# Kernel tuning notes

Measured on AMD Instinct MI355X. Metric: run time of the kernel, lower is better.

Reference implementation:

```python
import jax, jax.numpy as jnp
import numpy as np

N = 100_000      # nodes
E = 1_600_000    # edges
D = 128          # in_dim == hidden_dim
H = 4            # heads
HD = D // H      # per-head dim = 32
B = 8            # graphs in batch
TD = 128         # time_dim
NEG_SLOPE = 0.2
EPS = 1e-5


def _gelu(v):
    return jax.nn.gelu(v, approximate=False)  # torch default erf-GELU


def _layernorm(v, g, b):
    mu = jnp.mean(v, axis=-1, keepdims=True)
    var = jnp.var(v, axis=-1, keepdims=True)
    return (v - mu) * jax.lax.rsqrt(var + EPS) * g + b


def setup_inputs() -> dict:
    key = jax.random.key(0)
    ks = jax.random.split(key, 24)
    s = 1.0 / np.sqrt(D)
    inp = {
        "x": jax.random.normal(ks[0], (N, D), jnp.float32),
        "src": jax.random.randint(ks[1], (E,), 0, N),
        "dst": jax.random.randint(ks[2], (E,), 0, N),
        "graph_ids": jnp.sort(jax.random.randint(ks[3], (N,), 0, B)),
        "time_emb": jax.random.normal(ks[4], (B, TD), jnp.float32),
        # GATv2 params
        "Wsrc": jax.random.normal(ks[5], (D, D), jnp.float32) * s,
        "bsrc": jnp.zeros((D,), jnp.float32),
        "Wdst": jax.random.normal(ks[6], (D, D), jnp.float32) * s,
        "bdst": jnp.zeros((D,), jnp.float32),
        "attn": jax.random.normal(ks[7], (H, HD), jnp.float32) * (1.0 / np.sqrt(HD)),
        "gat_bias": jnp.zeros((D,), jnp.float32),
        # LayerNorms
        "ln1_g": jnp.ones((D,), jnp.float32), "ln1_b": jnp.zeros((D,), jnp.float32),
        "ln2_g": jnp.ones((D,), jnp.float32), "ln2_b": jnp.zeros((D,), jnp.float32),
        # time MLP
        "tW": jax.random.normal(ks[8], (TD, D), jnp.float32) * (1.0 / np.sqrt(TD)),
        "tb": jnp.zeros((D,), jnp.float32),
        # FFN
        "W1": jax.random.normal(ks[9], (D, 2 * D), jnp.float32) * s,
        "b1": jnp.zeros((2 * D,), jnp.float32),
        "W2": jax.random.normal(ks[10], (2 * D, D), jnp.float32) * (1.0 / np.sqrt(2 * D)),
        "b2": jnp.zeros((D,), jnp.float32),
    }
    return inp


def reference(x, src, dst, graph_ids, time_emb, Wsrc, bsrc, Wdst, bdst, attn,
              gat_bias, ln1_g, ln1_b, ln2_g, ln2_b, tW, tb, W1, b1, W2, b2):
    h = _layernorm(x, ln1_g, ln1_b)                       # [N, D]
    # GATv2Conv (share_weights=False, residual=False, activation=gelu)
    feat_src = (h @ Wsrc + bsrc).reshape(N, H, HD)        # [N, H, HD]
    feat_dst = (h @ Wdst + bdst).reshape(N, H, HD)
    e = feat_src[src] + feat_dst[dst]                     # [E, H, HD]
    e = jnp.where(e > 0, e, NEG_SLOPE * e)                # leaky_relu
    scores = jnp.einsum("ehd,hd->eh", e, attn)            # [E, H]
    # segment softmax over incoming edges of each dst node
    m = jax.ops.segment_max(scores, dst, num_segments=N)  # [N, H]
    ex = jnp.exp(scores - m[dst])
    denom = jax.ops.segment_sum(ex, dst, num_segments=N)  # [N, H]
    alpha = ex / denom[dst]                               # [E, H]
    msg = feat_src[src] * alpha[:, :, None]               # [E, H, HD]
    rst = jax.ops.segment_sum(msg, dst, num_segments=N)   # [N, H, HD]
    rst = _gelu(rst + gat_bias.reshape(H, HD))
    h = rst.reshape(N, D)                                 # flatten(1)
    # ragged time-embedding expand: time_condition[graph_of(node)]
    time_cond = _gelu(time_emb @ tW + tb)                 # [B, D]
    h = h + time_cond[graph_ids]
    h = h + x                                             # proj = Identity (in_dim == hidden_dim)
    h2 = _layernorm(h, ln2_g, ln2_b)
    h2 = _gelu(h2 @ W1 + b1) @ W2 + b2                    # FFN
    return h + h2
```

## Files before the change

### kernel.cpp

```cpp
#include <hip/hip_runtime.h>
#include <hip/hip_bf16.h>


#define RB 16
#define NEG_SLOPE 0.2f
#define LN_EPS 1e-5f

typedef __attribute__((ext_vector_type(8))) short short8v;
typedef __attribute__((ext_vector_type(4))) float floatx4;
typedef __attribute__((ext_vector_type(2))) float f32x2;

__device__ __forceinline__ float gelu_erf(float v) {
    return 0.5f * v * (1.0f + erff(v * 0.70710678118654752f));
}
__device__ __forceinline__ unsigned short f2bf(float f) {
    unsigned int u = __float_as_uint(f);
    u += 0x7fffu + ((u >> 16) & 1u);
    return (unsigned short)(u >> 16);
}

__device__ __forceinline__ void pack_region(
    const float* __restrict__ W, unsigned short* __restrict__ P, int K, int C, int idx)
{
    int total = (K >> 5) * (C >> 4) * 64;
    if (idx >= total) return;
    int lane = idx & 63;
    int f = idx >> 6;
    int nkt = K >> 5;
    int nt = f / nkt, kt = f - nt * nkt;
    int col = nt * 16 + (lane & 15);
    int k0 = kt * 32 + 8 * (lane >> 4);
    short8v v;
    #pragma unroll
    for (int i = 0; i < 8; ++i)
        v[i] = (short)f2bf(W[(size_t)(k0 + i) * C + col]);
    *(short8v*)(P + (size_t)idx * 8) = v;
}

__global__ __launch_bounds__(256) void prep(
    const float* __restrict__ temb, const float* __restrict__ tW,
    const float* __restrict__ tb, float* __restrict__ tc, int B,
    const float* __restrict__ Wsrc, unsigned short* __restrict__ pWs,
    const float* __restrict__ Wdst, unsigned short* __restrict__ pWd,
    const float* __restrict__ W1,   unsigned short* __restrict__ pW1,
    const float* __restrict__ W2,   unsigned short* __restrict__ pW2,
    int* __restrict__ deg, int N)
{
    const int bid = blockIdx.x;
    const int t   = threadIdx.x;
    if (bid == 0) {
        __shared__ float te[8 * 128];
        for (int i = t; i < B * 128; i += 256) te[i] = temb[i];
        __syncthreads();
        int c = t & 127, half = t >> 7;
        for (int b = half * 4; b < half * 4 + 4; ++b) {
            if (b >= B) break;
            float acc = 0.f;
            for (int k = 0; k < 128; ++k) acc = fmaf(te[b * 128 + k], tW[k * 128 + c], acc);
            tc[b * 128 + c] = gelu_erf(acc + tb[c]);
        }
    } else if (bid < 9) {
        pack_region(Wsrc, pWs, 128, 128, (bid - 1) * 256 + t);
    } else if (bid < 17) {
        pack_region(Wdst, pWd, 128, 128, (bid - 9) * 256 + t);
    } else if (bid < 33) {
        pack_region(W1, pW1, 128, 256, (bid - 17) * 256 + t);
    } else if (bid < 49) {
        pack_region(W2, pW2, 256, 128, (bid - 33) * 256 + t);
    } else {
        int idx = (bid - 49) * 1024 + t * 4;
        if (idx + 3 < N) {
            *(int4*)(deg + idx) = make_int4(0, 0, 0, 0);
        } else {
            if (idx     < N) deg[idx]     = 0;
            if (idx + 1 < N) deg[idx + 1] = 0;
            if (idx + 2 < N) deg[idx + 2] = 0;
            if (idx + 3 < N) deg[idx + 3] = 0;
        }
    }
}

__global__ __launch_bounds__(256) void csr_rank(
    const int* __restrict__ dst, int* __restrict__ deg, int* __restrict__ rank, int E)
{
    int e = blockIdx.x * 256 + threadIdx.x;
    if (e < E) rank[e] = atomicAdd(&deg[dst[e]], 1);
}

__global__ __launch_bounds__(256) void scan_blocks(
    const int* __restrict__ deg, int* __restrict__ rs, int* __restrict__ btot, int N)
{
    __shared__ int wtot[4];
    const int t    = threadIdx.x;
    const int idx  = blockIdx.x * 1024 + t * 4;
    int d0 = 0, d1 = 0, d2 = 0, d3 = 0;
    if (idx + 3 < N) {
        int4 v = *(const int4*)(deg + idx);
        d0 = v.x; d1 = v.y; d2 = v.z; d3 = v.w;
    } else {
        if (idx     < N) d0 = deg[idx];
        if (idx + 1 < N) d1 = deg[idx + 1];
        if (idx + 2 < N) d2 = deg[idx + 2];
        if (idx + 3 < N) d3 = deg[idx + 3];
    }
    const int ts = d0 + d1 + d2 + d3;
    const int lane = t & 63, w = t >> 6;
    int incl = ts;
    #pragma unroll
    for (int m = 1; m < 64; m <<= 1) { int u = __shfl_up(incl, m); if (lane >= m) incl += u; }
    if (lane == 63) wtot[w] = incl;
    __syncthreads();
    int woff = 0;
    #pragma unroll
    for (int i = 0; i < 4; ++i) woff += (i < w) ? wtot[i] : 0;
    const int p = woff + incl - ts;
    if (idx + 3 < N) {
        int4 o;
        o.x = p; o.y = p + d0; o.z = p + d0 + d1; o.w = p + d0 + d1 + d2;
        *(int4*)(rs + idx) = o;
    } else {
        if (idx     < N) rs[idx]     = p;
        if (idx + 1 < N) rs[idx + 1] = p + d0;
        if (idx + 2 < N) rs[idx + 2] = p + d0 + d1;
        if (idx + 3 < N) rs[idx + 3] = p + d0 + d1 + d2;
    }
    if (t == 255) btot[blockIdx.x] = woff + incl;
}

__global__ __launch_bounds__(64) void scan_tops(
    int* __restrict__ btot, int nb, int* __restrict__ rs, int N, int E)
{
    const int lane = threadIdx.x;
    int a0 = (2 * lane     < nb) ? btot[2 * lane]     : 0;
    int a1 = (2 * lane + 1 < nb) ? btot[2 * lane + 1] : 0;
    const int ts = a0 + a1;
    int incl = ts;
    #pragma unroll
    for (int m = 1; m < 64; m <<= 1) { int u = __shfl_up(incl, m); if (lane >= m) incl += u; }
    const int ex = incl - ts;
    if (2 * lane     < nb) btot[2 * lane]     = ex;
    if (2 * lane + 1 < nb) btot[2 * lane + 1] = ex + a0;
    if (lane == 0) rs[N] = E;
}

__global__ __launch_bounds__(256) void scan_add(
    int* __restrict__ rs, const int* __restrict__ btot, int N)
{
    int i = blockIdx.x * 256 + threadIdx.x;
    if (i < N) rs[i] += btot[i >> 10];
}

__global__ __launch_bounds__(256) void ln1_fill(
    const float* __restrict__ x,
    const float* __restrict__ ln_g, const float* __restrict__ ln_b,
    const unsigned short* __restrict__ pWs, const float* __restrict__ bsrc,
    const unsigned short* __restrict__ pWd, const float* __restrict__ bdst,
    unsigned short* __restrict__ fs, unsigned short* __restrict__ fdB, int nrows, int nLn1,
    const int* __restrict__ dst, const int* __restrict__ srcA,
    const int* __restrict__ rs, const int* __restrict__ rank,
    int* __restrict__ srcSorted, int E)
{
    __shared__ __align__(16) float hs[RB][132];
    __shared__ __align__(16) unsigned short pa[4 * 64 * 8];
    __shared__ float s_mu[RB], s_rs[RB];

    if (blockIdx.x >= nLn1) {
        int e = (blockIdx.x - nLn1) * 256 + threadIdx.x;
        if (e < E) srcSorted[rs[dst[e]] + rank[e]] = srcA[e];
        return;
    }

    const int tid  = threadIdx.x;
    const int row0 = blockIdx.x * RB;
    const int lane = tid & 63;
    const int w    = tid >> 6;

    #pragma unroll
    for (int i = 0; i < 2; ++i) {
        int f   = tid + i * 256;
        int row = f >> 5;
        int c0  = (f & 31) * 4;
        float4 v = make_float4(0.f, 0.f, 0.f, 0.f);
        if (row0 + row < nrows) v = *(const float4*)(x + (size_t)(row0 + row) * 128 + c0);
        *(float4*)&hs[row][c0] = v;
    }
    __syncthreads();

    {
        const int ln = lane;
        #pragma unroll
        for (int rr = 0; rr < 4; ++rr) {
            int row = w * 4 + rr;
            float v0 = hs[row][ln * 2], v1 = hs[row][ln * 2 + 1];
            float s = v0 + v1, sq = v0 * v0 + v1 * v1;
            #pragma unroll
            for (int m = 32; m; m >>= 1) { s += __shfl_xor(s, m); sq += __shfl_xor(sq, m); }
            if (ln == 0) {
                float mu  = s * (1.0f / 128.0f);
                float var = sq * (1.0f / 128.0f) - mu * mu;
                s_mu[row] = mu;
                s_rs[row] = rsqrtf(var + LN_EPS);
            }
        }
    }
    __syncthreads();

    {
        const int kt  = w;
        const int row = lane & 15;
        const int k0  = kt * 32 + 8 * (lane >> 4);
        float mu = s_mu[row], rs2 = s_rs[row];
        float4 u  = *(float4*)&hs[row][k0];
        float4 v  = *(float4*)&hs[row][k0 + 4];
        float4 g0 = *(const float4*)&ln_g[k0];
        float4 g1 = *(const float4*)&ln_g[k0 + 4];
        float4 c0 = *(const float4*)&ln_b[k0];
        float4 c1 = *(const float4*)&ln_b[k0 + 4];
        short8v pv;
        pv[0] = (short)f2bf((u.x - mu) * rs2 * g0.x + c0.x);
        pv[1] = (short)f2bf((u.y - mu) * rs2 * g0.y + c0.y);
        pv[2] = (short)f2bf((u.z - mu) * rs2 * g0.z + c0.z);
        pv[3] = (short)f2bf((u.w - mu) * rs2 * g0.w + c0.w);
        pv[4] = (short)f2bf((v.x - mu) * rs2 * g1.x + c1.x);
        pv[5] = (short)f2bf((v.y - mu) * rs2 * g1.y + c1.y);
        pv[6] = (short)f2bf((v.z - mu) * rs2 * g1.z + c1.z);
        pv[7] = (short)f2bf((v.w - mu) * rs2 * g1.w + c1.w);
        *(short8v*)&pa[(kt * 64 + lane) * 8] = pv;
    }
    __syncthreads();

    short8v a[4];
    #pragma unroll
    for (int kt = 0; kt < 4; ++kt)
        a[kt] = *(const short8v*)&pa[(kt * 64 + lane) * 8];

    #pragma unroll
    for (int j = 0; j < 2; ++j) {
        const int nt = 2 * w + j;
        floatx4 aS = {0.f, 0.f, 0.f, 0.f};
        floatx4 aD = {0.f, 0.f, 0.f, 0.f};
        #pragma unroll
        for (int kt = 0; kt < 4; ++kt) {
            short8v bS = *(const short8v*)(pWs + (size_t)((nt * 4 + kt) * 64 + lane) * 8);
            aS = __builtin_amdgcn_mfma_f32_16x16x32_bf16(a[kt], bS, aS, 0, 0, 0);
            short8v bD = *(const short8v*)(pWd + (size_t)((nt * 4 + kt) * 64 + lane) * 8);
            aD = __builtin_amdgcn_mfma_f32_16x16x32_bf16(a[kt], bD, aD, 0, 0, 0);
        }
        const int col = nt * 16 + (lane & 15);
        const float bS0 = bsrc[col], bD0 = bdst[col];
        #pragma unroll
        for (int r = 0; r < 4; ++r) {
            int grow = row0 + 4 * (lane >> 4) + r;
            if (grow < nrows) {
                fs [(size_t)grow * 128 + col] = f2bf(aS[r] + bS0);
                fdB[(size_t)grow * 128 + col] = f2bf(aD[r] + bD0);
            }
        }
    }
}

__global__ __launch_bounds__(256) void gat_gather(
    const unsigned short* __restrict__ fs, const unsigned short* __restrict__ fdB,
    float* __restrict__ hm, const float* __restrict__ x,
    const int* __restrict__ srcSorted, const int* __restrict__ rs,
    const float* __restrict__ attn, const float* __restrict__ gat_bias,
    const int* __restrict__ gid, const float* __restrict__ tc, int N)
{
    const int lane = threadIdx.x & 63;
    const int wib  = threadIdx.x >> 6;
    const int n    = blockIdx.x * 4 + wib;
    if (n >= N) return;

    const int g   = lane >> 4;
    const int l16 = lane & 15;
    const int d0  = l16 * 8;

    f32x2 c1v[4], c2v[4], vdv[4];
    {
        float4 a0 = *(const float4*)(attn + d0);
        float4 a1 = *(const float4*)(attn + d0 + 4);
        float av[8] = {a0.x, a0.y, a0.z, a0.w, a1.x, a1.y, a1.z, a1.w};
        uint4 vdu = *(const uint4*)(fdB + (size_t)n * 128 + d0);
        unsigned int uu[4] = {vdu.x, vdu.y, vdu.z, vdu.w};
        #pragma unroll
        for (int j = 0; j < 4; ++j) {
            c1v[j].x = 0.6f * av[2 * j];     c1v[j].y = 0.6f * av[2 * j + 1];
            c2v[j].x = 0.4f * av[2 * j];     c2v[j].y = 0.4f * av[2 * j + 1];
            vdv[j].x = __uint_as_float(uu[j] << 16);
            vdv[j].y = __uint_as_float(uu[j] & 0xffff0000u);
        }
    }

    const int lo = rs[n], hi = rs[n + 1];
    const int T  = (hi - lo + 3) >> 2;

    float den = 0.f;
    f32x2 wv[4] = {{0.f, 0.f}, {0.f, 0.f}, {0.f, 0.f}, {0.f, 0.f}};

    int i = lo + g;
    bool vA = (i < hi);
    int sA = vA ? srcSorted[i] : 0;
    uint4 rA = *(const uint4*)(fs + (size_t)sA * 128 + d0);

    for (int t = 0; t < T; ++t) {
        const int inx = i + 4;
        const bool vB = (inx < hi);
        const int sB = vB ? srcSorted[inx] : 0;
        uint4 rB = *(const uint4*)(fs + (size_t)sB * 128 + d0);

        unsigned int ru[4] = {rA.x, rA.y, rA.z, rA.w};
        f32x2 v2[4];
        #pragma unroll
        for (int j = 0; j < 4; ++j) {
            v2[j].x = __uint_as_float(ru[j] << 16);
            v2[j].y = __uint_as_float(ru[j] & 0xffff0000u);
        }

        f32x2 p2 = {0.f, 0.f};
        #pragma unroll
        for (int j = 0; j < 4; ++j) {
            f32x2 e = v2[j] + vdv[j];
            p2 = __builtin_elementwise_fma(c1v[j], e, p2);
            p2 = __builtin_elementwise_fma(c2v[j],
                     __builtin_elementwise_abs(e), p2);
        }
        float p = p2.x + p2.y;
        p += __shfl_xor(p, 1);
        p += __shfl_xor(p, 2);
        float exv = vA ? __expf(p) : 0.f;
        den += exv;
        f32x2 ex2; ex2.x = exv; ex2.y = exv;
        #pragma unroll
        for (int j = 0; j < 4; ++j)
            wv[j] = __builtin_elementwise_fma(ex2, v2[j], wv[j]);

        vA = vB; rA = rB; i = inx;
    }

    float w[8];
    #pragma unroll
    for (int j = 0; j < 4; ++j) { w[2 * j] = wv[j].x; w[2 * j + 1] = wv[j].y; }

    den += __shfl_xor(den, 16);
    den += __shfl_xor(den, 32);
    #pragma unroll
    for (int j = 0; j < 8; ++j) {
        w[j] += __shfl_xor(w[j], 16);
        w[j] += __shfl_xor(w[j], 32);
    }

    if (g == 0) {
        const float inv = den > 0.f ? 1.0f / den : 0.f;
        const int gg = gid[n];
        float4 x0 = *(const float4*)(x  + (size_t)n * 128 + d0);
        float4 x1 = *(const float4*)(x  + (size_t)n * 128 + d0 + 4);
        float4 t0 = *(const float4*)(tc + (size_t)gg * 128 + d0);
        float4 t1 = *(const float4*)(tc + (size_t)gg * 128 + d0 + 4);
        float4 g0 = *(const float4*)(gat_bias + d0);
        float4 g1 = *(const float4*)(gat_bias + d0 + 4);
        float4 o0, o1;
        o0.x = gelu_erf(w[0] * inv + g0.x) + t0.x + x0.x;
        o0.y = gelu_erf(w[1] * inv + g0.y) + t0.y + x0.y;
        o0.z = gelu_erf(w[2] * inv + g0.z) + t0.z + x0.z;
        o0.w = gelu_erf(w[3] * inv + g0.w) + t0.w + x0.w;
        o1.x = gelu_erf(w[4] * inv + g1.x) + t1.x + x1.x;
        o1.y = gelu_erf(w[5] * inv + g1.y) + t1.y + x1.y;
        o1.z = gelu_erf(w[6] * inv + g1.z) + t1.z + x1.z;
        o1.w = gelu_erf(w[7] * inv + g1.w) + t1.w + x1.w;
        *(float4*)(hm + (size_t)n * 128 + d0)     = o0;
        *(float4*)(hm + (size_t)n * 128 + d0 + 4) = o1;
    }
}

__global__ __launch_bounds__(256) void combine_ffn(
    const float* __restrict__ hmg,
    const float* __restrict__ ln_g, const float* __restrict__ ln_b,
    const unsigned short* __restrict__ pW1, const float* __restrict__ b1,
    const unsigned short* __restrict__ pW2, const float* __restrict__ b2,
    float* __restrict__ out, int nrows)
{
    __shared__ __align__(16) float hs[RB][132];
    __shared__ __align__(16) unsigned short pa[4 * 64 * 8];
    __shared__ __align__(16) unsigned short a2[RB * 264];
    __shared__ float s_mu[RB], s_rs[RB];

    const int tid  = threadIdx.x;
    const int row0 = blockIdx.x * RB;
    const int lane = tid & 63;
    const int w    = tid >> 6;

    #pragma unroll
    for (int i = 0; i < 2; ++i) {
        int f   = tid + i * 256;
        int row = f >> 5;
        int c0  = (f & 31) * 4;
        float4 v = make_float4(0.f, 0.f, 0.f, 0.f);
        if (row0 + row < nrows) v = *(const float4*)(hmg + (size_t)(row0 + row) * 128 + c0);
        *(float4*)&hs[row][c0] = v;
    }
    __syncthreads();

    {
        const int ln = lane;
        #pragma unroll
        for (int rr = 0; rr < 4; ++rr) {
            int row = w * 4 + rr;
            float v0 = hs[row][ln * 2], v1 = hs[row][ln * 2 + 1];
            float s = v0 + v1, sq = v0 * v0 + v1 * v1;
            #pragma unroll
            for (int m = 32; m; m >>= 1) { s += __shfl_xor(s, m); sq += __shfl_xor(sq, m); }
            if (ln == 0) {
                float mu  = s * (1.0f / 128.0f);
                float var = sq * (1.0f / 128.0f) - mu * mu;
                s_mu[row] = mu;
                s_rs[row] = rsqrtf(var + LN_EPS);
            }
        }
    }
    __syncthreads();

    {
        const int kt  = w;
        const int row = lane & 15;
        const int k0  = kt * 32 + 8 * (lane >> 4);
        float mu = s_mu[row], rs2 = s_rs[row];
        float4 u  = *(float4*)&hs[row][k0];
        float4 v  = *(float4*)&hs[row][k0 + 4];
        float4 g0 = *(const float4*)&ln_g[k0];
        float4 g1 = *(const float4*)&ln_g[k0 + 4];
        float4 c0 = *(const float4*)&ln_b[k0];
        float4 c1 = *(const float4*)&ln_b[k0 + 4];
        short8v pv;
        pv[0] = (short)f2bf((u.x - mu) * rs2 * g0.x + c0.x);
        pv[1] = (short)f2bf((u.y - mu) * rs2 * g0.y + c0.y);
        pv[2] = (short)f2bf((u.z - mu) * rs2 * g0.z + c0.z);
        pv[3] = (short)f2bf((u.w - mu) * rs2 * g0.w + c0.w);
        pv[4] = (short)f2bf((v.x - mu) * rs2 * g1.x + c1.x);
        pv[5] = (short)f2bf((v.y - mu) * rs2 * g1.y + c1.y);
        pv[6] = (short)f2bf((v.z - mu) * rs2 * g1.z + c1.z);
        pv[7] = (short)f2bf((v.w - mu) * rs2 * g1.w + c1.w);
        *(short8v*)&pa[(kt * 64 + lane) * 8] = pv;
    }
    __syncthreads();

    {
        short8v a[4];
        #pragma unroll
        for (int kt = 0; kt < 4; ++kt)
            a[kt] = *(const short8v*)&pa[(kt * 64 + lane) * 8];

        #pragma unroll
        for (int jj = 0; jj < 4; ++jj) {
            const int nt = 4 * w + jj;
            floatx4 acc = {0.f, 0.f, 0.f, 0.f};
            #pragma unroll
            for (int kt = 0; kt < 4; ++kt) {
                short8v b = *(const short8v*)(pW1 + (size_t)((nt * 4 + kt) * 64 + lane) * 8);
                acc = __builtin_amdgcn_mfma_f32_16x16x32_bf16(a[kt], b, acc, 0, 0, 0);
            }
            const int col = nt * 16 + (lane & 15);
            const float bb = b1[col];
            #pragma unroll
            for (int r = 0; r < 4; ++r) {
                int rowD = 4 * (lane >> 4) + r;
                a2[rowD * 264 + col] = f2bf(gelu_erf(acc[r] + bb));
            }
        }
    }
    __syncthreads();

    {
        floatx4 acc2[2] = {{0.f, 0.f, 0.f, 0.f}, {0.f, 0.f, 0.f, 0.f}};
        #pragma unroll
        for (int kt = 0; kt < 8; ++kt) {
            short8v af = *(const short8v*)&a2[(lane & 15) * 264 + kt * 32 + 8 * (lane >> 4)];
            #pragma unroll
            for (int j = 0; j < 2; ++j) {
                const int nt = 2 * w + j;
                short8v b = *(const short8v*)(pW2 + (size_t)((nt * 8 + kt) * 64 + lane) * 8);
                acc2[j] = __builtin_amdgcn_mfma_f32_16x16x32_bf16(af, b, acc2[j], 0, 0, 0);
            }
        }
        #pragma unroll
        for (int j = 0; j < 2; ++j) {
            const int col = (2 * w + j) * 16 + (lane & 15);
            const float bb = b2[col];
            #pragma unroll
            for (int r = 0; r < 4; ++r) {
                int rowD = 4 * (lane >> 4) + r;
                int grow = row0 + rowD;
                if (grow < nrows)
                    out[(size_t)grow * 128 + col] = hs[rowD][col] + acc2[j][r] + bb;
            }
        }
    }
}

extern "C" void kernel_launch(void* const* d_in, const int* in_sizes, int n_in,
                              void* d_out, int out_size, void* d_ws, size_t ws_size,
                              hipStream_t stream)
{
    const float* x    = (const float*)d_in[0];
    const int*   src  = (const int*)  d_in[1];
    const int*   dst  = (const int*)  d_in[2];
    const int*   gid  = (const int*)  d_in[3];
    const float* temb = (const float*)d_in[4];
    const float* Wsrc = (const float*)d_in[5];
    const float* bsrc = (const float*)d_in[6];
    const float* Wdst = (const float*)d_in[7];
    const float* bdst = (const float*)d_in[8];
    const float* attn = (const float*)d_in[9];
    const float* gbias= (const float*)d_in[10];
    const float* ln1g = (const float*)d_in[11];
    const float* ln1b = (const float*)d_in[12];
    const float* ln2g = (const float*)d_in[13];
    const float* ln2b = (const float*)d_in[14];
    const float* tW   = (const float*)d_in[15];
    const float* tb   = (const float*)d_in[16];
    const float* W1   = (const float*)d_in[17];
    const float* b1   = (const float*)d_in[18];
    const float* W2   = (const float*)d_in[19];
    const float* b2   = (const float*)d_in[20];

    const int N = in_sizes[0] / 128;
    const int E = in_sizes[1];
    const int B = in_sizes[4] / 128;
    float* out = (float*)d_out;

    char* ws = (char*)d_ws;
    size_t off = 0;
    auto alloc = [&](size_t bytes) { void* p = ws + off; off += (bytes + 255) & ~(size_t)255; return p; };
    unsigned short* fs  = (unsigned short*)alloc((size_t)N * 128 * 2);
    unsigned short* fdB = (unsigned short*)alloc((size_t)N * 128 * 2);
    float* hm           = (float*)         alloc((size_t)N * 128 * 4);
    int*   deg          = (int*)           alloc((size_t)N * 4);
    int*   rsb          = (int*)           alloc((size_t)(N + 1) * 4);
    int*   rank         = (int*)           alloc((size_t)E * 4);
    int*   srcSorted    = (int*)           alloc((size_t)E * 4);
    float* tc           = (float*)         alloc((size_t)B * 128 * 4);
    int*   btot         = (int*)           alloc((size_t)1024 * 4);
    unsigned short* pWs = (unsigned short*)alloc((size_t)128 * 128 * 2);
    unsigned short* pWd = (unsigned short*)alloc((size_t)128 * 128 * 2);
    unsigned short* pW1 = (unsigned short*)alloc((size_t)128 * 256 * 2);
    unsigned short* pW2 = (unsigned short*)alloc((size_t)256 * 128 * 2);

    const int nbScan = (N + 1023) >> 10;
    const int nbZero = (N + 1023) >> 10;
    const int nLn1   = (N + RB - 1) / RB;
    const int nFill  = (E + 255) / 256;

    prep<<<49 + nbZero, 256, 0, stream>>>(temb, tW, tb, tc, B,
        Wsrc, pWs, Wdst, pWd, W1, pW1, W2, pW2, deg, N);
    csr_rank<<<(E + 255) / 256, 256, 0, stream>>>(dst, deg, rank, E);
    scan_blocks<<<nbScan, 256, 0, stream>>>(deg, rsb, btot, N);
    scan_tops<<<1, 64, 0, stream>>>(btot, nbScan, rsb, N, E);
    scan_add<<<(N + 255) / 256, 256, 0, stream>>>(rsb, btot, N);
    ln1_fill<<<nLn1 + nFill, 256, 0, stream>>>(
        x, ln1g, ln1b, pWs, bsrc, pWd, bdst, fs, fdB, N, nLn1,
        dst, src, rsb, rank, srcSorted, E);
    gat_gather<<<(N + 3) / 4, 256, 0, stream>>>(
        fs, fdB, hm, x, srcSorted, rsb, attn, gbias, gid, tc, N);
    combine_ffn<<<(N + RB - 1) / RB, 256, 0, stream>>>(
        hm, ln2g, ln2b, pW1, b1, pW2, b2, out, N);
}
```

Baseline: 270.0 us.

## Fuse GAT gather into FFN kernel and merge CSR rank into prep

Merges the per-node attention gather with the LayerNorm+FFN kernel, so each block gathers its 16 rows straight into shared memory instead of writing and re-reading a full fp32 intermediate. It also folds the edge-rank atomic pass into the prep launch and zeroes the degree array with a memset instead of prep blocks. This cuts one N×128 fp32 round trip to global memory and one kernel launch. In exchange, each wave now processes 4 nodes serially, and the gather has fewer waves in flight to hide latency.

```diff
diff --git a/kernel.cpp b/kernel.cpp
--- a/kernel.cpp
+++ b/kernel.cpp
@@ -38,16 +38,22 @@
 }
 
 __global__ __launch_bounds__(256) void prep(
+    const int* __restrict__ dst, int* __restrict__ deg, int* __restrict__ rank,
+    int E, int nRank,
     const float* __restrict__ temb, const float* __restrict__ tW,
     const float* __restrict__ tb, float* __restrict__ tc, int B,
     const float* __restrict__ Wsrc, unsigned short* __restrict__ pWs,
     const float* __restrict__ Wdst, unsigned short* __restrict__ pWd,
     const float* __restrict__ W1,   unsigned short* __restrict__ pW1,
-    const float* __restrict__ W2,   unsigned short* __restrict__ pW2,
-    int* __restrict__ deg, int N)
-{
-    const int bid = blockIdx.x;
-    const int t   = threadIdx.x;
+    const float* __restrict__ W2,   unsigned short* __restrict__ pW2)
+{
+    const int t = threadIdx.x;
+    if (blockIdx.x < nRank) {
+        int e = blockIdx.x * 256 + t;
+        if (e < E) rank[e] = atomicAdd(&deg[dst[e]], 1);
+        return;
+    }
+    const int bid = blockIdx.x - nRank;
     if (bid == 0) {
         __shared__ float te[8 * 128];
         for (int i = t; i < B * 128; i += 256) te[i] = temb[i];
@@ -65,26 +71,9 @@
         pack_region(Wdst, pWd, 128, 128, (bid - 9) * 256 + t);
     } else if (bid < 33) {
         pack_region(W1, pW1, 128, 256, (bid - 17) * 256 + t);
-    } else if (bid < 49) {
+    } else {
         pack_region(W2, pW2, 256, 128, (bid - 33) * 256 + t);
-    } else {
-        int idx = (bid - 49) * 1024 + t * 4;
-        if (idx + 3 < N) {
-            *(int4*)(deg + idx) = make_int4(0, 0, 0, 0);
-        } else {
-            if (idx     < N) deg[idx]     = 0;
-            if (idx + 1 < N) deg[idx + 1] = 0;
-            if (idx + 2 < N) deg[idx + 2] = 0;
-            if (idx + 3 < N) deg[idx + 3] = 0;
-        }
-    }
-}
-
-__global__ __launch_bounds__(256) void csr_rank(
-    const int* __restrict__ dst, int* __restrict__ deg, int* __restrict__ rank, int E)
-{
-    int e = blockIdx.x * 256 + threadIdx.x;
-    if (e < E) rank[e] = atomicAdd(&deg[dst[e]], 1);
+    }
 }
 
 __global__ __launch_bounds__(256) void scan_blocks(
@@ -259,125 +248,16 @@
     }
 }
 
-__global__ __launch_bounds__(256) void gat_gather(
+__global__ __launch_bounds__(256) void gather_ffn(
     const unsigned short* __restrict__ fs, const unsigned short* __restrict__ fdB,
-    float* __restrict__ hm, const float* __restrict__ x,
+    const float* __restrict__ x,
     const int* __restrict__ srcSorted, const int* __restrict__ rs,
     const float* __restrict__ attn, const float* __restrict__ gat_bias,
-    const int* __restrict__ gid, const float* __restrict__ tc, int N)
-{
-    const int lane = threadIdx.x & 63;
-    const int wib  = threadIdx.x >> 6;
-    const int n    = blockIdx.x * 4 + wib;
-    if (n >= N) return;
-
-    const int g   = lane >> 4;
-    const int l16 = lane & 15;
-    const int d0  = l16 * 8;
-
-    f32x2 c1v[4], c2v[4], vdv[4];
-    {
-        float4 a0 = *(const float4*)(attn + d0);
-        float4 a1 = *(const float4*)(attn + d0 + 4);
-        float av[8] = {a0.x, a0.y, a0.z, a0.w, a1.x, a1.y, a1.z, a1.w};
-        uint4 vdu = *(const uint4*)(fdB + (size_t)n * 128 + d0);
-        unsigned int uu[4] = {vdu.x, vdu.y, vdu.z, vdu.w};
-        #pragma unroll
-        for (int j = 0; j < 4; ++j) {
-            c1v[j].x = 0.6f * av[2 * j];     c1v[j].y = 0.6f * av[2 * j + 1];
-            c2v[j].x = 0.4f * av[2 * j];     c2v[j].y = 0.4f * av[2 * j + 1];
-            vdv[j].x = __uint_as_float(uu[j] << 16);
-            vdv[j].y = __uint_as_float(uu[j] & 0xffff0000u);
-        }
-    }
-
-    const int lo = rs[n], hi = rs[n + 1];
-    const int T  = (hi - lo + 3) >> 2;
-
-    float den = 0.f;
-    f32x2 wv[4] = {{0.f, 0.f}, {0.f, 0.f}, {0.f, 0.f}, {0.f, 0.f}};
-
-    int i = lo + g;
-    bool vA = (i < hi);
-    int sA = vA ? srcSorted[i] : 0;
-    uint4 rA = *(const uint4*)(fs + (size_t)sA * 128 + d0);
-
-    for (int t = 0; t < T; ++t) {
-        const int inx = i + 4;
-        const bool vB = (inx < hi);
-        const int sB = vB ? srcSorted[inx] : 0;
-        uint4 rB = *(const uint4*)(fs + (size_t)sB * 128 + d0);
-
-        unsigned int ru[4] = {rA.x, rA.y, rA.z, rA.w};
-        f32x2 v2[4];
-        #pragma unroll
-        for (int j = 0; j < 4; ++j) {
-            v2[j].x = __uint_as_float(ru[j] << 16);
-            v2[j].y = __uint_as_float(ru[j] & 0xffff0000u);
-        }
-
-        f32x2 p2 = {0.f, 0.f};
-        #pragma unroll
-        for (int j = 0; j < 4; ++j) {
-            f32x2 e = v2[j] + vdv[j];
-            p2 = __builtin_elementwise_fma(c1v[j], e, p2);
-            p2 = __builtin_elementwise_fma(c2v[j],
-                     __builtin_elementwise_abs(e), p2);
-        }
-        float p = p2.x + p2.y;
-        p += __shfl_xor(p, 1);
-        p += __shfl_xor(p, 2);
-        float exv = vA ? __expf(p) : 0.f;
-        den += exv;
-        f32x2 ex2; ex2.x = exv; ex2.y = exv;
-        #pragma unroll
-        for (int j = 0; j < 4; ++j)
-            wv[j] = __builtin_elementwise_fma(ex2, v2[j], wv[j]);
-
-        vA = vB; rA = rB; i = inx;
-    }
-
-    float w[8];
-    #pragma unroll
-    for (int j = 0; j < 4; ++j) { w[2 * j] = wv[j].x; w[2 * j + 1] = wv[j].y; }
-
-    den += __shfl_xor(den, 16);
-    den += __shfl_xor(den, 32);
-    #pragma unroll
-    for (int j = 0; j < 8; ++j) {
-        w[j] += __shfl_xor(w[j], 16);
-        w[j] += __shfl_xor(w[j], 32);
-    }
-
-    if (g == 0) {
-        const float inv = den > 0.f ? 1.0f / den : 0.f;
-        const int gg = gid[n];
-        float4 x0 = *(const float4*)(x  + (size_t)n * 128 + d0);
-        float4 x1 = *(const float4*)(x  + (size_t)n * 128 + d0 + 4);
-        float4 t0 = *(const float4*)(tc + (size_t)gg * 128 + d0);
-        float4 t1 = *(const float4*)(tc + (size_t)gg * 128 + d0 + 4);
-        float4 g0 = *(const float4*)(gat_bias + d0);
-        float4 g1 = *(const float4*)(gat_bias + d0 + 4);
-        float4 o0, o1;
-        o0.x = gelu_erf(w[0] * inv + g0.x) + t0.x + x0.x;
-        o0.y = gelu_erf(w[1] * inv + g0.y) + t0.y + x0.y;
-        o0.z = gelu_erf(w[2] * inv + g0.z) + t0.z + x0.z;
-        o0.w = gelu_erf(w[3] * inv + g0.w) + t0.w + x0.w;
-        o1.x = gelu_erf(w[4] * inv + g1.x) + t1.x + x1.x;
-        o1.y = gelu_erf(w[5] * inv + g1.y) + t1.y + x1.y;
-        o1.z = gelu_erf(w[6] * inv + g1.z) + t1.z + x1.z;
-        o1.w = gelu_erf(w[7] * inv + g1.w) + t1.w + x1.w;
-        *(float4*)(hm + (size_t)n * 128 + d0)     = o0;
-        *(float4*)(hm + (size_t)n * 128 + d0 + 4) = o1;
-    }
-}
-
-__global__ __launch_bounds__(256) void combine_ffn(
-    const float* __restrict__ hmg,
+    const int* __restrict__ gid, const float* __restrict__ tc,
     const float* __restrict__ ln_g, const float* __restrict__ ln_b,
     const unsigned short* __restrict__ pW1, const float* __restrict__ b1,
     const unsigned short* __restrict__ pW2, const float* __restrict__ b2,
-    float* __restrict__ out, int nrows)
+    float* __restrict__ out, int N)
 {
     __shared__ __align__(16) float hs[RB][132];
     __shared__ __align__(16) unsigned short pa[4 * 64 * 8];
@@ -389,14 +269,124 @@
     const int lane = tid & 63;
     const int w    = tid >> 6;
 
-    #pragma unroll
-    for (int i = 0; i < 2; ++i) {
-        int f   = tid + i * 256;
-        int row = f >> 5;
-        int c0  = (f & 31) * 4;
-        float4 v = make_float4(0.f, 0.f, 0.f, 0.f);
-        if (row0 + row < nrows) v = *(const float4*)(hmg + (size_t)(row0 + row) * 128 + c0);
-        *(float4*)&hs[row][c0] = v;
+    const int g   = lane >> 4;
+    const int l16 = lane & 15;
+    const int d0  = l16 * 8;
+
+    f32x2 c1v[4], c2v[4];
+    {
+        float4 a0 = *(const float4*)(attn + d0);
+        float4 a1 = *(const float4*)(attn + d0 + 4);
+        float av[8] = {a0.x, a0.y, a0.z, a0.w, a1.x, a1.y, a1.z, a1.w};
+        #pragma unroll
+        for (int j = 0; j < 4; ++j) {
+            c1v[j].x = 0.6f * av[2 * j];  c1v[j].y = 0.6f * av[2 * j + 1];
+            c2v[j].x = 0.4f * av[2 * j];  c2v[j].y = 0.4f * av[2 * j + 1];
+        }
+    }
+
+    for (int nn = 0; nn < 4; ++nn) {
+        const int row = w * 4 + nn;
+        const int n   = row0 + row;
+        if (n >= N) {
+            if (g == 0) {
+                float4 z = make_float4(0.f, 0.f, 0.f, 0.f);
+                *(float4*)&hs[row][d0]     = z;
+                *(float4*)&hs[row][d0 + 4] = z;
+            }
+            continue;
+        }
+
+        f32x2 vdv[4];
+        {
+            uint4 vdu = *(const uint4*)(fdB + (size_t)n * 128 + d0);
+            unsigned int uu[4] = {vdu.x, vdu.y, vdu.z, vdu.w};
+            #pragma unroll
+            for (int j = 0; j < 4; ++j) {
+                vdv[j].x = __uint_as_float(uu[j] << 16);
+                vdv[j].y = __uint_as_float(uu[j] & 0xffff0000u);
+            }
+        }
+
+        const int lo = rs[n], hi = rs[n + 1];
+        const int T  = (hi - lo + 3) >> 2;
+
+        float den = 0.f;
+        f32x2 wv[4] = {{0.f, 0.f}, {0.f, 0.f}, {0.f, 0.f}, {0.f, 0.f}};
+
+        int i = lo + g;
+        bool vA = (i < hi);
+        int sA = vA ? srcSorted[i] : 0;
+        uint4 rA = *(const uint4*)(fs + (size_t)sA * 128 + d0);
+
+        for (int t = 0; t < T; ++t) {
+            const int inx = i + 4;
+            const bool vB = (inx < hi);
+            const int sB = vB ? srcSorted[inx] : 0;
+            uint4 rB = *(const uint4*)(fs + (size_t)sB * 128 + d0);
+
+            unsigned int ru[4] = {rA.x, rA.y, rA.z, rA.w};
+            f32x2 v2[4];
+            #pragma unroll
+            for (int j = 0; j < 4; ++j) {
+                v2[j].x = __uint_as_float(ru[j] << 16);
+                v2[j].y = __uint_as_float(ru[j] & 0xffff0000u);
+            }
+
+            f32x2 p2 = {0.f, 0.f};
+            #pragma unroll
+            for (int j = 0; j < 4; ++j) {
+                f32x2 e = v2[j] + vdv[j];
+                p2 = __builtin_elementwise_fma(c1v[j], e, p2);
+                p2 = __builtin_elementwise_fma(c2v[j],
+                         __builtin_elementwise_abs(e), p2);
+            }
+            float p = p2.x + p2.y;
+            p += __shfl_xor(p, 1);
+            p += __shfl_xor(p, 2);
+            float exv = vA ? __expf(p) : 0.f;
+            den += exv;
+            f32x2 ex2; ex2.x = exv; ex2.y = exv;
+            #pragma unroll
+            for (int j = 0; j < 4; ++j)
+                wv[j] = __builtin_elementwise_fma(ex2, v2[j], wv[j]);
+
+            vA = vB; rA = rB; i = inx;
+        }
+
+        float ww[8];
+        #pragma unroll
+        for (int j = 0; j < 4; ++j) { ww[2 * j] = wv[j].x; ww[2 * j + 1] = wv[j].y; }
+
+        den += __shfl_xor(den, 16);
+        den += __shfl_xor(den, 32);
+        #pragma unroll
+        for (int j = 0; j < 8; ++j) {
+            ww[j] += __shfl_xor(ww[j], 16);
+            ww[j] += __shfl_xor(ww[j], 32);
+        }
+
+        if (g == 0) {
+            const float inv = den > 0.f ? 1.0f / den : 0.f;
+            const int gg = gid[n];
+            float4 x0 = *(const float4*)(x  + (size_t)n * 128 + d0);
+            float4 x1 = *(const float4*)(x  + (size_t)n * 128 + d0 + 4);
+            float4 t0 = *(const float4*)(tc + (size_t)gg * 128 + d0);
+            float4 t1 = *(const float4*)(tc + (size_t)gg * 128 + d0 + 4);
+            float4 g0 = *(const float4*)(gat_bias + d0);
+            float4 g1 = *(const float4*)(gat_bias + d0 + 4);
+            float4 o0, o1;
+            o0.x = gelu_erf(ww[0] * inv + g0.x) + t0.x + x0.x;
+            o0.y = gelu_erf(ww[1] * inv + g0.y) + t0.y + x0.y;
+            o0.z = gelu_erf(ww[2] * inv + g0.z) + t0.z + x0.z;
+            o0.w = gelu_erf(ww[3] * inv + g0.w) + t0.w + x0.w;
+            o1.x = gelu_erf(ww[4] * inv + g1.x) + t1.x + x1.x;
+            o1.y = gelu_erf(ww[5] * inv + g1.y) + t1.y + x1.y;
+            o1.z = gelu_erf(ww[6] * inv + g1.z) + t1.z + x1.z;
+            o1.w = gelu_erf(ww[7] * inv + g1.w) + t1.w + x1.w;
+            *(float4*)&hs[row][d0]     = o0;
+            *(float4*)&hs[row][d0 + 4] = o1;
+        }
     }
     __syncthreads();
 
@@ -489,7 +479,7 @@
             for (int r = 0; r < 4; ++r) {
                 int rowD = 4 * (lane >> 4) + r;
                 int grow = row0 + rowD;
-                if (grow < nrows)
+                if (grow < N)
                     out[(size_t)grow * 128 + col] = hs[rowD][col] + acc2[j][r] + bb;
             }
         }
@@ -532,7 +522,6 @@
     auto alloc = [&](size_t bytes) { void* p = ws + off; off += (bytes + 255) & ~(size_t)255; return p; };
     unsigned short* fs  = (unsigned short*)alloc((size_t)N * 128 * 2);
     unsigned short* fdB = (unsigned short*)alloc((size_t)N * 128 * 2);
-    float* hm           = (float*)         alloc((size_t)N * 128 * 4);
     int*   deg          = (int*)           alloc((size_t)N * 4);
     int*   rsb          = (int*)           alloc((size_t)(N + 1) * 4);
     int*   rank         = (int*)           alloc((size_t)E * 4);
@@ -545,21 +534,20 @@
     unsigned short* pW2 = (unsigned short*)alloc((size_t)256 * 128 * 2);
 
     const int nbScan = (N + 1023) >> 10;
-    const int nbZero = (N + 1023) >> 10;
+    const int nRank  = (E + 255) / 256;
     const int nLn1   = (N + RB - 1) / RB;
     const int nFill  = (E + 255) / 256;
 
-    prep<<<49 + nbZero, 256, 0, stream>>>(temb, tW, tb, tc, B,
-        Wsrc, pWs, Wdst, pWd, W1, pW1, W2, pW2, deg, N);
-    csr_rank<<<(E + 255) / 256, 256, 0, stream>>>(dst, deg, rank, E);
+    hipMemsetAsync(deg, 0, (size_t)N * 4, stream);
+    prep<<<nRank + 49, 256, 0, stream>>>(dst, deg, rank, E, nRank,
+        temb, tW, tb, tc, B, Wsrc, pWs, Wdst, pWd, W1, pW1, W2, pW2);
     scan_blocks<<<nbScan, 256, 0, stream>>>(deg, rsb, btot, N);
     scan_tops<<<1, 64, 0, stream>>>(btot, nbScan, rsb, N, E);
     scan_add<<<(N + 255) / 256, 256, 0, stream>>>(rsb, btot, N);
     ln1_fill<<<nLn1 + nFill, 256, 0, stream>>>(
         x, ln1g, ln1b, pWs, bsrc, pWd, bdst, fs, fdB, N, nLn1,
         dst, src, rsb, rank, srcSorted, E);
-    gat_gather<<<(N + 3) / 4, 256, 0, stream>>>(
-        fs, fdB, hm, x, srcSorted, rsb, attn, gbias, gid, tc, N);
-    combine_ffn<<<(N + RB - 1) / RB, 256, 0, stream>>>(
-        hm, ln2g, ln2b, pW1, b1, pW2, b2, out, N);
-}
+    gather_ffn<<<(N + RB - 1) / RB, 256, 0, stream>>>(
+        fs, fdB, x, srcSorted, rsb, attn, gbias, gid, tc,
+        ln2g, ln2b, pW1, b1, pW2, b2, out, N);
+}
```

Result: slower. 286.0 us (+5.9%).

## Store GAT output intermediate in bf16 and fuse rank into prep kernel

Applied to the files above, without the earlier changes.

The gather kernel now writes its combined output (GAT result plus time embedding plus residual) as packed bf16 instead of fp32, and the FFN kernel unpacks it into shared memory. This halves the memory traffic for that intermediate. The degree zeroing moves to a memset and the edge-rank atomic pass is merged into the prep kernel, removing one launch. The risk is reduced precision on the residual stream, which feeds the final output.

```diff
diff --git a/kernel.cpp b/kernel.cpp
--- a/kernel.cpp
+++ b/kernel.cpp
@@ -17,6 +17,9 @@
     unsigned int u = __float_as_uint(f);
     u += 0x7fffu + ((u >> 16) & 1u);
     return (unsigned short)(u >> 16);
+}
+__device__ __forceinline__ float bf2f(unsigned short u) {
+    return __uint_as_float(((unsigned int)u) << 16);
 }
 
 __device__ __forceinline__ void pack_region(
@@ -38,16 +41,22 @@
 }
 
 __global__ __launch_bounds__(256) void prep(
+    const int* __restrict__ dst, int* __restrict__ deg, int* __restrict__ rank,
+    int E, int nRank,
     const float* __restrict__ temb, const float* __restrict__ tW,
     const float* __restrict__ tb, float* __restrict__ tc, int B,
     const float* __restrict__ Wsrc, unsigned short* __restrict__ pWs,
     const float* __restrict__ Wdst, unsigned short* __restrict__ pWd,
     const float* __restrict__ W1,   unsigned short* __restrict__ pW1,
-    const float* __restrict__ W2,   unsigned short* __restrict__ pW2,
-    int* __restrict__ deg, int N)
-{
-    const int bid = blockIdx.x;
-    const int t   = threadIdx.x;
+    const float* __restrict__ W2,   unsigned short* __restrict__ pW2)
+{
+    const int t = threadIdx.x;
+    if (blockIdx.x < nRank) {
+        int e = blockIdx.x * 256 + t;
+        if (e < E) rank[e] = atomicAdd(&deg[dst[e]], 1);
+        return;
+    }
+    const int bid = blockIdx.x - nRank;
     if (bid == 0) {
         __shared__ float te[8 * 128];
         for (int i = t; i < B * 128; i += 256) te[i] = temb[i];
@@ -65,26 +74,9 @@
         pack_region(Wdst, pWd, 128, 128, (bid - 9) * 256 + t);
     } else if (bid < 33) {
         pack_region(W1, pW1, 128, 256, (bid - 17) * 256 + t);
-    } else if (bid < 49) {
+    } else {
         pack_region(W2, pW2, 256, 128, (bid - 33) * 256 + t);
-    } else {
-        int idx = (bid - 49) * 1024 + t * 4;
-        if (idx + 3 < N) {
-            *(int4*)(deg + idx) = make_int4(0, 0, 0, 0);
-        } else {
-            if (idx     < N) deg[idx]     = 0;
-            if (idx + 1 < N) deg[idx + 1] = 0;
-            if (idx + 2 < N) deg[idx + 2] = 0;
-            if (idx + 3 < N) deg[idx + 3] = 0;
-        }
-    }
-}
-
-__global__ __launch_bounds__(256) void csr_rank(
-    const int* __restrict__ dst, int* __restrict__ deg, int* __restrict__ rank, int E)
-{
-    int e = blockIdx.x * 256 + threadIdx.x;
-    if (e < E) rank[e] = atomicAdd(&deg[dst[e]], 1);
+    }
 }
 
 __global__ __launch_bounds__(256) void scan_blocks(
@@ -261,7 +253,7 @@
 
 __global__ __launch_bounds__(256) void gat_gather(
     const unsigned short* __restrict__ fs, const unsigned short* __restrict__ fdB,
-    float* __restrict__ hm, const float* __restrict__ x,
+    unsigned short* __restrict__ hm, const float* __restrict__ x,
     const int* __restrict__ srcSorted, const int* __restrict__ rs,
     const float* __restrict__ attn, const float* __restrict__ gat_bias,
     const int* __restrict__ gid, const float* __restrict__ tc, int N)
@@ -358,22 +350,26 @@
         float4 t1 = *(const float4*)(tc + (size_t)gg * 128 + d0 + 4);
         float4 g0 = *(const float4*)(gat_bias + d0);
         float4 g1 = *(const float4*)(gat_bias + d0 + 4);
-        float4 o0, o1;
-        o0.x = gelu_erf(w[0] * inv + g0.x) + t0.x + x0.x;
-        o0.y = gelu_erf(w[1] * inv + g0.y) + t0.y + x0.y;
-        o0.z = gelu_erf(w[2] * inv + g0.z) + t0.z + x0.z;
-        o0.w = gelu_erf(w[3] * inv + g0.w) + t0.w + x0.w;
-        o1.x = gelu_erf(w[4] * inv + g1.x) + t1.x + x1.x;
-        o1.y = gelu_erf(w[5] * inv + g1.y) + t1.y + x1.y;
-        o1.z = gelu_erf(w[6] * inv + g1.z) + t1.z + x1.z;
-        o1.w = gelu_erf(w[7] * inv + g1.w) + t1.w + x1.w;
-        *(float4*)(hm + (size_t)n * 128 + d0)     = o0;
-        *(float4*)(hm + (size_t)n * 128 + d0 + 4) = o1;
+        float o[8];
+        o[0] = gelu_erf(w[0] * inv + g0.x) + t0.x + x0.x;
+        o[1] = gelu_erf(w[1] * inv + g0.y) + t0.y + x0.y;
+        o[2] = gelu_erf(w[2] * inv + g0.z) + t0.z + x0.z;
+        o[3] = gelu_erf(w[3] * inv + g0.w) + t0.w + x0.w;
+        o[4] = gelu_erf(w[4] * inv + g1.x) + t1.x + x1.x;
+        o[5] = gelu_erf(w[5] * inv + g1.y) + t1.y + x1.y;
+        o[6] = gelu_erf(w[6] * inv + g1.z) + t1.z + x1.z;
+        o[7] = gelu_erf(w[7] * inv + g1.w) + t1.w + x1.w;
+        uint4 pk;
+        pk.x = (unsigned int)f2bf(o[0]) | ((unsigned int)f2bf(o[1]) << 16);
+        pk.y = (unsigned int)f2bf(o[2]) | ((unsigned int)f2bf(o[3]) << 16);
+        pk.z = (unsigned int)f2bf(o[4]) | ((unsigned int)f2bf(o[5]) << 16);
+        pk.w = (unsigned int)f2bf(o[6]) | ((unsigned int)f2bf(o[7]) << 16);
+        *(uint4*)(hm + (size_t)n * 128 + d0) = pk;
     }
 }
 
 __global__ __launch_bounds__(256) void combine_ffn(
-    const float* __restrict__ hmg,
+    const unsigned short* __restrict__ hmg,
     const float* __restrict__ ln_g, const float* __restrict__ ln_b,
     const unsigned short* __restrict__ pW1, const float* __restrict__ b1,
     const unsigned short* __restrict__ pW2, const float* __restrict__ b2,
@@ -389,14 +385,20 @@
     const int lane = tid & 63;
     const int w    = tid >> 6;
 
-    #pragma unroll
-    for (int i = 0; i < 2; ++i) {
-        int f   = tid + i * 256;
-        int row = f >> 5;
-        int c0  = (f & 31) * 4;
-        float4 v = make_float4(0.f, 0.f, 0.f, 0.f);
-        if (row0 + row < nrows) v = *(const float4*)(hmg + (size_t)(row0 + row) * 128 + c0);
-        *(float4*)&hs[row][c0] = v;
+    {
+        int row = tid >> 4;
+        int c0  = (tid & 15) * 8;
+        uint4 u = make_uint4(0, 0, 0, 0);
+        if (row0 + row < nrows) u = *(const uint4*)(hmg + (size_t)(row0 + row) * 128 + c0);
+        float* hr = &hs[row][c0];
+        hr[0] = __uint_as_float(u.x << 16);
+        hr[1] = __uint_as_float(u.x & 0xffff0000u);
+        hr[2] = __uint_as_float(u.y << 16);
+        hr[3] = __uint_as_float(u.y & 0xffff0000u);
+        hr[4] = __uint_as_float(u.z << 16);
+        hr[5] = __uint_as_float(u.z & 0xffff0000u);
+        hr[6] = __uint_as_float(u.w << 16);
+        hr[7] = __uint_as_float(u.w & 0xffff0000u);
     }
     __syncthreads();
 
@@ -532,7 +534,7 @@
     auto alloc = [&](size_t bytes) { void* p = ws + off; off += (bytes + 255) & ~(size_t)255; return p; };
     unsigned short* fs  = (unsigned short*)alloc((size_t)N * 128 * 2);
     unsigned short* fdB = (unsigned short*)alloc((size_t)N * 128 * 2);
-    float* hm           = (float*)         alloc((size_t)N * 128 * 4);
+    unsigned short* hm  = (unsigned short*)alloc((size_t)N * 128 * 2);
     int*   deg          = (int*)           alloc((size_t)N * 4);
     int*   rsb          = (int*)           alloc((size_t)(N + 1) * 4);
     int*   rank         = (int*)           alloc((size_t)E * 4);
@@ -545,13 +547,13 @@
     unsigned short* pW2 = (unsigned short*)alloc((size_t)256 * 128 * 2);
 
     const int nbScan = (N + 1023) >> 10;
-    const int nbZero = (N + 1023) >> 10;
+    const int nRank  = (E + 255) / 256;
     const int nLn1   = (N + RB - 1) / RB;
     const int nFill  = (E + 255) / 256;
 
-    prep<<<49 + nbZero, 256, 0, stream>>>(temb, tW, tb, tc, B,
-        Wsrc, pWs, Wdst, pWd, W1, pW1, W2, pW2, deg, N);
-    csr_rank<<<(E + 255) / 256, 256, 0, stream>>>(dst, deg, rank, E);
+    hipMemsetAsync(deg, 0, (size_t)N * 4, stream);
+    prep<<<nRank + 49, 256, 0, stream>>>(dst, deg, rank, E, nRank,
+        temb, tW, tb, tc, B, Wsrc, pWs, Wdst, pWd, W1, pW1, W2, pW2);
     scan_blocks<<<nbScan, 256, 0, stream>>>(deg, rsb, btot, N);
     scan_tops<<<1, 64, 0, stream>>>(btot, nbScan, rsb, N, E);
     scan_add<<<(N + 255) / 256, 256, 0, stream>>>(rsb, btot, N);
```

Measured after the change: 264.1 us. -2.2%, faster.
